# Kernel optimization log

Hardware: AMD Instinct MI355X
Metric: run time of the kernel (lower is better)

The kernel has to match this reference:

```python
import jax, jax.numpy as jnp
import numpy as np

B, S, E, H = 8, 2048, 512, 8
DH = E // H
NEG = -1e30


def setup_inputs() -> dict:
    key = jax.random.key(0)
    ks = jax.random.split(key, 6)
    return {
        "x": jax.random.normal(ks[0], (B, S, E), dtype=jnp.float32),
        "W_qkv": jax.random.normal(ks[1], (E, 3 * E), dtype=jnp.float32) * 0.02,
        "b_qkv": jax.random.normal(ks[2], (3 * E,), dtype=jnp.float32) * 0.02,
        "W_out": jax.random.normal(ks[3], (E, E), dtype=jnp.float32) * 0.02,
        "b_out": jax.random.normal(ks[4], (E,), dtype=jnp.float32) * 0.02,
        "rel_pos": jax.random.normal(ks[5], (1, H, S, S), dtype=jnp.float32) * 0.02,
    }


def reference(x, W_qkv, b_qkv, W_out, b_out, rel_pos):
    b, s, e = x.shape
    scale = DH ** -0.5
    qkv = x @ W_qkv + b_qkv                     # [b, s, 3e]
    qkv = qkv.reshape(b, s, 3, H, DH)
    q = jnp.transpose(qkv[:, :, 0], (0, 2, 1, 3))  # [b, h, s, dh]
    k = jnp.transpose(qkv[:, :, 1], (0, 2, 1, 3))
    v = jnp.transpose(qkv[:, :, 2], (0, 2, 1, 3))
    scores = jnp.einsum("bhqd,bhkd->bhqk", q, k) * scale
    scores = scores + rel_pos[:, :, :s, :s]
    causal = jnp.tril(jnp.ones((s, s), dtype=bool))
    scores = jnp.where(causal[None, None], scores, NEG)
    attn = jax.nn.softmax(scores, axis=-1)
    out = jnp.einsum("bhqk,bhkd->bhqd", attn, v)  # [b, h, s, dh]
    out = jnp.transpose(out, (0, 2, 1, 3)).reshape(b, s, e)
    return out @ W_out + b_out
```

## Files before the change

kernel.cpp:

```cpp
#include <hip/hip_runtime.h>
#include <cstdint>


#define DEVI __device__ __forceinline__

typedef __bf16 bf8 __attribute__((ext_vector_type(8)));
typedef float f4 __attribute__((ext_vector_type(4)));
typedef unsigned short us8 __attribute__((ext_vector_type(8)));
typedef unsigned short us4 __attribute__((ext_vector_type(4)));

typedef const unsigned int __attribute__((address_space(1))) gu32;
typedef unsigned int __attribute__((address_space(3))) lu32;

#define L2E 1.44269504088896f

DEVI unsigned short f2bf(float f) {
  unsigned u = __builtin_bit_cast(unsigned, f);
  u += 0x7fffu + ((u >> 16) & 1u);
  return (unsigned short)(u >> 16);
}

DEVI unsigned short cbf(float f) {
  return __builtin_bit_cast(unsigned short, (__bf16)f);
}

DEVI void gl_lds16(const void* g, void* l) {
  __builtin_amdgcn_global_load_lds((gu32*)g, (lu32*)l, 16, 0, 0);
}

__global__ __launch_bounds__(256) void k_convert_x(const float* __restrict__ x,
                                                   unsigned short* __restrict__ xb) {
  int c = blockIdx.x * 256 + threadIdx.x;
  int row = c >> 6, cl = c & 63;
  const float* s = x + ((size_t)row << 9) + (cl << 3);
  float4 a = *(const float4*)s;
  float4 b = *(const float4*)(s + 4);
  us8 o;
  o[0]=f2bf(a.x); o[1]=f2bf(a.y); o[2]=f2bf(a.z); o[3]=f2bf(a.w);
  o[4]=f2bf(b.x); o[5]=f2bf(b.y); o[6]=f2bf(b.z); o[7]=f2bf(b.w);
  int p = (cl & ~7) | ((cl & 7) ^ (row & 7));
  *(us8*)(xb + ((size_t)row << 9) + (p << 3)) = o;
}

__global__ __launch_bounds__(256) void k_transpose_w(const float* __restrict__ W,
                                                     unsigned short* __restrict__ Wt, int N) {
  __shared__ float t[32][33];
  int k0 = blockIdx.x * 32, n0 = blockIdx.y * 32;
  int tx = threadIdx.x & 31, ty = threadIdx.x >> 5;
#pragma unroll
  for (int r = 0; r < 4; ++r)
    t[ty + r * 8][tx] = W[(size_t)(k0 + ty + r * 8) * N + n0 + tx];
  __syncthreads();
#pragma unroll
  for (int r = 0; r < 4; ++r) {
    int n = n0 + ty + r * 8, k = k0 + tx;
    int k2 = (k & ~63) | ((((k >> 3) & 7) ^ (n & 7)) << 3) | (k & 7);
    Wt[((size_t)n << 9) + k2] = f2bf(t[tx][ty + r * 8]);
  }
}

__global__ __launch_bounds__(256) void k_relconv(const float* __restrict__ rel,
                                                 unsigned short* __restrict__ relt) {
  int t = blockIdx.x * 256 + threadIdx.x;
  int lane = t & 63, ct = (t >> 6) & 3, kt = (t >> 8) & 31, q16 = (t >> 13) & 127, h = t >> 20;
  if (kt > (q16 >> 2)) return;
  int row = (q16 << 4) + (lane & 15);
  int col = (kt << 6) + (ct << 4) + ((lane >> 4) << 2);
  float4 v = *(const float4*)(rel + ((size_t)h << 22) + ((size_t)row << 11) + col);
  us4 o;
  o[0] = f2bf(v.x * L2E); o[1] = f2bf(v.y * L2E);
  o[2] = f2bf(v.z * L2E); o[3] = f2bf(v.w * L2E);
  size_t idx = ((((((size_t)h << 7) | q16) << 5) | kt) << 2 | ct) << 6 | lane;
  *(us4*)(relt + (idx << 2)) = o;
}

template <int EPI>
__global__ __launch_bounds__(256, 2)
void k_gemm(const unsigned short* __restrict__ Ag, const unsigned short* __restrict__ Bg,
            const float* __restrict__ bias, float* __restrict__ Of,
            unsigned short* __restrict__ Oq, unsigned short* __restrict__ Ok,
            unsigned short* __restrict__ Ov) {
  __shared__ __align__(16) unsigned short lds[128 * 64 * 2];
  unsigned short* Al = lds;
  unsigned short* Bl = lds + 128 * 64;
  const int tid = threadIdx.x, wv = tid >> 6, lane = tid & 63, g = lane >> 4, cl = lane & 15;
  const int wm = wv >> 1, wn = wv & 1;
  const int row0 = blockIdx.x * 128, col0 = blockIdx.y * 128;
  f4 acc[4][4];
#pragma unroll
  for (int i = 0; i < 4; ++i)
#pragma unroll
    for (int j = 0; j < 4; ++j) acc[i][j] = (f4){0.f, 0.f, 0.f, 0.f};

  for (int kt = 0; kt < 8; ++kt) {
#pragma unroll
    for (int j = 0; j < 4; ++j) {
      int ci = wv * 4 + j;
      int gci = ci * 64 + lane;
      int r = gci >> 3, cc = gci & 7;
      gl_lds16(Ag + ((size_t)(row0 + r) << 9) + kt * 64 + cc * 8, Al + ci * 512);
      gl_lds16(Bg + ((size_t)(col0 + r) << 9) + kt * 64 + cc * 8, Bl + ci * 512);
    }
    __syncthreads();
#pragma unroll
    for (int kk = 0; kk < 2; ++kk) {
      bf8 af[4], bb[4];
#pragma unroll
      for (int mf = 0; mf < 4; ++mf) {
        int r = wm * 64 + mf * 16 + cl;
        int cc = (kk * 4 + g) ^ (r & 7);
        af[mf] = *(const bf8*)(Al + r * 64 + cc * 8);
      }
#pragma unroll
      for (int nf = 0; nf < 4; ++nf) {
        int r = wn * 64 + nf * 16 + cl;
        int cc = (kk * 4 + g) ^ (r & 7);
        bb[nf] = *(const bf8*)(Bl + r * 64 + cc * 8);
      }
#pragma unroll
      for (int mf = 0; mf < 4; ++mf)
#pragma unroll
        for (int nf = 0; nf < 4; ++nf)
          acc[mf][nf] = __builtin_amdgcn_mfma_f32_16x16x32_bf16(af[mf], bb[nf], acc[mf][nf], 0, 0, 0);
    }
    __syncthreads();
  }

  if (EPI == 1) {
#pragma unroll
    for (int nf = 0; nf < 4; ++nf) {
      int col = col0 + wn * 64 + nf * 16 + cl;
      float bv = bias[col];
#pragma unroll
      for (int mf = 0; mf < 4; ++mf) {
#pragma unroll
        for (int j = 0; j < 4; ++j) {
          int row = row0 + wm * 64 + mf * 16 + 4 * g + j;
          Of[((size_t)row << 9) + col] = acc[mf][nf][j] + bv;
        }
      }
    }
  } else {
    const int which = col0 >> 9;
#pragma unroll
    for (int nf = 0; nf < 4; ++nf) {
      int col = col0 + wn * 64 + nf * 16 + cl;
      float bv = bias[col];
      int d = col & 63, h = (col >> 6) & 7;
#pragma unroll
      for (int mf = 0; mf < 4; ++mf) {
        int row = row0 + wm * 64 + mf * 16 + 4 * g;
        int b = row >> 11, s = row & 2047;
        size_t fb = ((size_t)b * 8 + h) * 131072;
        if (which == 0) {
#pragma unroll
          for (int j = 0; j < 4; ++j) {
            int ss = s + j;
            size_t off = fb + (size_t)((ss >> 4) * 1024 + (d >> 5) * 512 +
                                       (((d >> 3) & 3) * 16 + (ss & 15)) * 8 + (d & 7));
            Oq[off] = f2bf((acc[mf][nf][j] + bv) * (0.125f * L2E));
          }
        } else if (which == 1) {
#pragma unroll
          for (int j = 0; j < 4; ++j) {
            int ss = s + j;
            size_t off = fb + (size_t)((ss >> 6) * 4096 + (d >> 5) * 2048 + ((ss >> 4) & 3) * 512 +
                                       (((d >> 3) & 3) * 16 + (ss & 15)) * 8 + (d & 7));
            Ok[off] = f2bf(acc[mf][nf][j] + bv);
          }
        } else {
          us4 o;
#pragma unroll
          for (int j = 0; j < 4; ++j) o[j] = f2bf(acc[mf][nf][j] + bv);
          size_t off = fb + (size_t)((s >> 6) * 4096 + ((s >> 5) & 1) * 2048 + (d >> 4) * 512 +
                                     ((((s >> 3) & 3) * 16) + (d & 15)) * 8 + (s & 7));
          *(us4*)(Ov + off) = o;
        }
      }
    }
  }
}

template <bool RELT>
__global__ __launch_bounds__(256, 4)
void k_attn(const unsigned short* __restrict__ Qf, const unsigned short* __restrict__ Kf,
            const unsigned short* __restrict__ Vf, const float* __restrict__ rel,
            const unsigned short* __restrict__ relt, unsigned short* __restrict__ AO) {
  __shared__ __align__(16) unsigned short Pl[4][16 * 72];
  const int tid = threadIdx.x, wv = tid >> 6, lane = tid & 63, g = lane >> 4, cl = lane & 15;
  int bid = blockIdx.x;
  int h = bid & 7;
  int rest = bid >> 3;
  int q16 = 127 - (rest >> 1);
  int b = ((rest & 1) << 2) | wv;
  const int rX = q16 << 4;
  const int ktop = q16 >> 2;
  const int qrow = rX + cl;
  size_t fb = (((size_t)b << 3) + h) * 131072;
  const unsigned short* Qp = Qf + fb;
  const unsigned short* Kp = Kf + fb;
  const unsigned short* Vp = Vf + fb;
  const float* relp = rel + ((size_t)h << 22);
  unsigned short* pw = Pl[wv];

  bf8 qf[2];
#pragma unroll
  for (int kk = 0; kk < 2; ++kk)
    qf[kk] = *(const bf8*)(Qp + q16 * 1024 + kk * 512 + lane * 8);

  f4 ot[4];
  float mr = -1e30f, lr = 0.f;
#pragma unroll
  for (int ct = 0; ct < 4; ++ct) ot[ct] = (f4){0.f, 0.f, 0.f, 0.f};

  for (int kt = 0; kt <= ktop; ++kt) {
    const int kb = kt << 6;
    const unsigned short* Kt = Kp + kt * 4096;
    const unsigned short* Vt = Vp + kt * 4096;
    bf8 kf[2][4], vf[2][4];
#pragma unroll
    for (int kk = 0; kk < 2; ++kk)
#pragma unroll
      for (int ct = 0; ct < 4; ++ct)
        kf[kk][ct] = *(const bf8*)(Kt + kk * 2048 + ct * 512 + lane * 8);
#pragma unroll
    for (int kk = 0; kk < 2; ++kk)
#pragma unroll
      for (int ct = 0; ct < 4; ++ct)
        vf[kk][ct] = *(const bf8*)(Vt + kk * 2048 + ct * 512 + lane * 8);
    us4 rt4[4];
    float4 rl4[4];
    if constexpr (RELT) {
      const unsigned short* tb = relt + (((((size_t)h << 7) | q16) << 5) | kt) * 1024;
#pragma unroll
      for (int ct = 0; ct < 4; ++ct)
        rt4[ct] = *(const us4*)(tb + ((ct << 6) | lane) * 4);
    } else {
#pragma unroll
      for (int ct = 0; ct < 4; ++ct)
        rl4[ct] = *(const float4*)(relp + ((size_t)qrow << 11) + kb + ct * 16 + g * 4);
    }
    f4 st[4];
#pragma unroll
    for (int ct = 0; ct < 4; ++ct) st[ct] = (f4){0.f, 0.f, 0.f, 0.f};
#pragma unroll
    for (int kk = 0; kk < 2; ++kk)
#pragma unroll
      for (int ct = 0; ct < 4; ++ct)
        st[ct] = __builtin_amdgcn_mfma_f32_16x16x32_bf16(kf[kk][ct], qf[kk], st[ct], 0, 0, 0);
    if constexpr (RELT) {
#pragma unroll
      for (int ct = 0; ct < 4; ++ct)
#pragma unroll
        for (int j = 0; j < 4; ++j)
          st[ct][j] += __builtin_bit_cast(float, (unsigned)rt4[ct][j] << 16);
    } else {
#pragma unroll
      for (int ct = 0; ct < 4; ++ct) {
        st[ct][0] = fmaf(rl4[ct].x, L2E, st[ct][0]);
        st[ct][1] = fmaf(rl4[ct].y, L2E, st[ct][1]);
        st[ct][2] = fmaf(rl4[ct].z, L2E, st[ct][2]);
        st[ct][3] = fmaf(rl4[ct].w, L2E, st[ct][3]);
      }
    }
    if (kt == ktop) {
#pragma unroll
      for (int ct = 0; ct < 4; ++ct) {
        int kc0 = kb + ct * 16 + 4 * g;
#pragma unroll
        for (int j = 0; j < 4; ++j)
          if (kc0 + j > qrow) st[ct][j] = -1e30f;
      }
    }
    float m0 = fmaxf(fmaxf(st[0][0], st[0][1]), fmaxf(st[0][2], st[0][3]));
#pragma unroll
    for (int ct = 1; ct < 4; ++ct)
      m0 = fmaxf(m0, fmaxf(fmaxf(st[ct][0], st[ct][1]), fmaxf(st[ct][2], st[ct][3])));
    m0 = fmaxf(m0, __shfl_xor(m0, 16));
    m0 = fmaxf(m0, __shfl_xor(m0, 32));
    float mn = fmaxf(mr, m0);
    float al = exp2f(mr - mn);
    mr = mn;
#pragma unroll
    for (int ct = 0; ct < 4; ++ct)
#pragma unroll
      for (int j = 0; j < 4; ++j) st[ct][j] = exp2f(st[ct][j] - mn);
    float rs = 0.f;
#pragma unroll
    for (int ct = 0; ct < 4; ++ct)
      rs += (st[ct][0] + st[ct][1]) + (st[ct][2] + st[ct][3]);
    rs += __shfl_xor(rs, 16);
    rs += __shfl_xor(rs, 32);
    lr = lr * al + rs;
#pragma unroll
    for (int ct = 0; ct < 4; ++ct) {
      ot[ct][0] *= al; ot[ct][1] *= al; ot[ct][2] *= al; ot[ct][3] *= al;
    }
#pragma unroll
    for (int ct = 0; ct < 4; ++ct) {
      us4 pk;
      pk[0] = cbf(st[ct][0]); pk[1] = cbf(st[ct][1]);
      pk[2] = cbf(st[ct][2]); pk[3] = cbf(st[ct][3]);
      *(us4*)(pw + cl * 72 + ct * 16 + g * 4) = pk;
    }
#pragma unroll
    for (int kk = 0; kk < 2; ++kk) {
      bf8 pf = __builtin_bit_cast(bf8, *(const us8*)(pw + cl * 72 + kk * 32 + g * 8));
#pragma unroll
      for (int ct = 0; ct < 4; ++ct)
        ot[ct] = __builtin_amdgcn_mfma_f32_16x16x32_bf16(vf[kk][ct], pf, ot[ct], 0, 0, 0);
    }
  }
  float inv = 1.0f / lr;
  const int s = qrow;
  unsigned short* aor = AO + (((size_t)b << 11) + s) * 512 + h * 64;
#pragma unroll
  for (int ct = 0; ct < 4; ++ct) {
    int chunk = 2 * ct + (g >> 1);
    int base = (4 * (g & 1)) | ((chunk ^ (s & 7)) << 3);
    us4 o;
    o[0] = cbf(ot[ct][0] * inv); o[1] = cbf(ot[ct][1] * inv);
    o[2] = cbf(ot[ct][2] * inv); o[3] = cbf(ot[ct][3] * inv);
    *(us4*)(aor + base) = o;
  }
}

extern "C" void kernel_launch(void* const* d_in, const int* in_sizes, int n_in,
                              void* d_out, int out_size, void* d_ws, size_t ws_size,
                              hipStream_t stream) {
  const float* x    = (const float*)d_in[0];
  const float* Wqkv = (const float*)d_in[1];
  const float* bqkv = (const float*)d_in[2];
  const float* Wout = (const float*)d_in[3];
  const float* bout = (const float*)d_in[4];
  const float* rel  = (const float*)d_in[5];
  float* out = (float*)d_out;

  unsigned short* Qw  = (unsigned short*)d_ws;
  unsigned short* Kw  = Qw  + 8388608;
  unsigned short* Vw  = Kw  + 8388608;
  unsigned short* XA  = Vw  + 8388608;
  unsigned short* WtQ = XA  + 8388608;
  unsigned short* WtO = WtQ + 786432;
  unsigned short* relt= WtO + 262144;
  const bool useT = ws_size >= (34603008ULL + 33554432ULL) * 2ULL;

  k_convert_x<<<dim3(4096), dim3(256), 0, stream>>>(x, XA);
  k_transpose_w<<<dim3(16, 48), dim3(256), 0, stream>>>(Wqkv, WtQ, 1536);
  k_transpose_w<<<dim3(16, 16), dim3(256), 0, stream>>>(Wout, WtO, 512);
  if (useT) k_relconv<<<dim3(32768), dim3(256), 0, stream>>>(rel, relt);
  k_gemm<0><<<dim3(128, 12), dim3(256), 0, stream>>>(XA, WtQ, bqkv, nullptr, Qw, Kw, Vw);
  if (useT) k_attn<true ><<<dim3(2048), dim3(256), 0, stream>>>(Qw, Kw, Vw, rel, relt, XA);
  else      k_attn<false><<<dim3(2048), dim3(256), 0, stream>>>(Qw, Kw, Vw, rel, relt, XA);
  k_gemm<1><<<dim3(128, 4), dim3(256), 0, stream>>>(XA, WtO, bout, out, nullptr, nullptr, nullptr);
}
```

Measured before the change: 199.7 us.

## Coalesce rel-pos conversion via LDS, lazy softmax rescale, swizzle P tile

The rel-pos conversion kernel now has each wave read full contiguous 64-float row segments, stage them through shared memory and write the MFMA-fragment layout, replacing scattered float4 reads. In attention, the running-max rescale of the accumulator and row sum is skipped unless some row's max grows by more than a threshold, which saves exp and multiply work per tile. Scores are then exponentiated against a possibly stale max, which can reach up to about 2^11.5 but stays finite. The P staging buffer drops its padding and uses an XOR swizzle to avoid LDS bank conflicts.

```diff
diff --git a/kernel.cpp b/kernel.cpp
--- a/kernel.cpp
+++ b/kernel.cpp
@@ -61,17 +61,30 @@
 
 __global__ __launch_bounds__(256) void k_relconv(const float* __restrict__ rel,
                                                  unsigned short* __restrict__ relt) {
-  int t = blockIdx.x * 256 + threadIdx.x;
-  int lane = t & 63, ct = (t >> 6) & 3, kt = (t >> 8) & 31, q16 = (t >> 13) & 127, h = t >> 20;
+  __shared__ __align__(16) float tl[4][16][68];
+  int wv = threadIdx.x >> 6, lane = threadIdx.x & 63;
+  int t = blockIdx.x * 4 + wv;
+  int kt = t & 31, q16 = (t >> 5) & 127, h = t >> 12;
   if (kt > (q16 >> 2)) return;
-  int row = (q16 << 4) + (lane & 15);
-  int col = (kt << 6) + (ct << 4) + ((lane >> 4) << 2);
-  float4 v = *(const float4*)(rel + ((size_t)h << 22) + ((size_t)row << 11) + col);
-  us4 o;
-  o[0] = f2bf(v.x * L2E); o[1] = f2bf(v.y * L2E);
-  o[2] = f2bf(v.z * L2E); o[3] = f2bf(v.w * L2E);
-  size_t idx = ((((((size_t)h << 7) | q16) << 5) | kt) << 2 | ct) << 6 | lane;
-  *(us4*)(relt + (idx << 2)) = o;
+  const float* src = rel + ((size_t)h << 22) +
+                     ((size_t)((q16 << 4) + (lane >> 2)) << 11) + (kt << 6) + (lane & 3) * 16;
+  float4 v0 = *(const float4*)(src);
+  float4 v1 = *(const float4*)(src + 4);
+  float4 v2 = *(const float4*)(src + 8);
+  float4 v3 = *(const float4*)(src + 12);
+  float* dst = &tl[wv][lane >> 2][(lane & 3) * 16];
+  *(float4*)(dst) = v0; *(float4*)(dst + 4) = v1;
+  *(float4*)(dst + 8) = v2; *(float4*)(dst + 12) = v3;
+  size_t tb = (((((size_t)h << 7) | q16) << 5) | kt) << 2;
+#pragma unroll
+  for (int ct = 0; ct < 4; ++ct) {
+    const float* rp = &tl[wv][lane & 15][ct * 16 + ((lane >> 4) << 2)];
+    float4 rv = *(const float4*)rp;
+    us4 o;
+    o[0] = f2bf(rv.x * L2E); o[1] = f2bf(rv.y * L2E);
+    o[2] = f2bf(rv.z * L2E); o[3] = f2bf(rv.w * L2E);
+    *(us4*)(relt + (((tb | ct) << 6) | lane) * 4) = o;
+  }
 }
 
 template <int EPI>
@@ -186,7 +199,7 @@
 void k_attn(const unsigned short* __restrict__ Qf, const unsigned short* __restrict__ Kf,
             const unsigned short* __restrict__ Vf, const float* __restrict__ rel,
             const unsigned short* __restrict__ relt, unsigned short* __restrict__ AO) {
-  __shared__ __align__(16) unsigned short Pl[4][16 * 72];
+  __shared__ __align__(16) unsigned short Pl[4][16 * 64];
   const int tid = threadIdx.x, wv = tid >> 6, lane = tid & 63, g = lane >> 4, cl = lane & 15;
   int bid = blockIdx.x;
   int h = bid & 7;
@@ -278,34 +291,38 @@
       m0 = fmaxf(m0, fmaxf(fmaxf(st[ct][0], st[ct][1]), fmaxf(st[ct][2], st[ct][3])));
     m0 = fmaxf(m0, __shfl_xor(m0, 16));
     m0 = fmaxf(m0, __shfl_xor(m0, 32));
-    float mn = fmaxf(mr, m0);
-    float al = exp2f(mr - mn);
-    mr = mn;
+    if (__any(m0 > mr + 11.54f)) {
+      float mn = fmaxf(mr, m0);
+      float al = exp2f(mr - mn);
+      mr = mn;
+      lr *= al;
+#pragma unroll
+      for (int ct = 0; ct < 4; ++ct) {
+        ot[ct][0] *= al; ot[ct][1] *= al; ot[ct][2] *= al; ot[ct][3] *= al;
+      }
+    }
 #pragma unroll
     for (int ct = 0; ct < 4; ++ct)
 #pragma unroll
-      for (int j = 0; j < 4; ++j) st[ct][j] = exp2f(st[ct][j] - mn);
+      for (int j = 0; j < 4; ++j) st[ct][j] = exp2f(st[ct][j] - mr);
     float rs = 0.f;
 #pragma unroll
     for (int ct = 0; ct < 4; ++ct)
       rs += (st[ct][0] + st[ct][1]) + (st[ct][2] + st[ct][3]);
     rs += __shfl_xor(rs, 16);
     rs += __shfl_xor(rs, 32);
-    lr = lr * al + rs;
-#pragma unroll
-    for (int ct = 0; ct < 4; ++ct) {
-      ot[ct][0] *= al; ot[ct][1] *= al; ot[ct][2] *= al; ot[ct][3] *= al;
-    }
+    lr += rs;
 #pragma unroll
     for (int ct = 0; ct < 4; ++ct) {
       us4 pk;
       pk[0] = cbf(st[ct][0]); pk[1] = cbf(st[ct][1]);
       pk[2] = cbf(st[ct][2]); pk[3] = cbf(st[ct][3]);
-      *(us4*)(pw + cl * 72 + ct * 16 + g * 4) = pk;
+      *(us4*)(pw + cl * 64 + (((2 * ct + (g >> 1)) ^ (cl & 7)) << 3) + ((g & 1) << 2)) = pk;
     }
 #pragma unroll
     for (int kk = 0; kk < 2; ++kk) {
-      bf8 pf = __builtin_bit_cast(bf8, *(const us8*)(pw + cl * 72 + kk * 32 + g * 8));
+      bf8 pf = __builtin_bit_cast(bf8,
+                 *(const us8*)(pw + cl * 64 + (((4 * kk + g) ^ (cl & 7)) << 3)));
 #pragma unroll
       for (int ct = 0; ct < 4; ++ct)
         ot[ct] = __builtin_amdgcn_mfma_f32_16x16x32_bf16(vf[kk][ct], pf, ot[ct], 0, 0, 0);
@@ -348,7 +365,7 @@
   k_convert_x<<<dim3(4096), dim3(256), 0, stream>>>(x, XA);
   k_transpose_w<<<dim3(16, 48), dim3(256), 0, stream>>>(Wqkv, WtQ, 1536);
   k_transpose_w<<<dim3(16, 16), dim3(256), 0, stream>>>(Wout, WtO, 512);
-  if (useT) k_relconv<<<dim3(32768), dim3(256), 0, stream>>>(rel, relt);
+  if (useT) k_relconv<<<dim3(8192), dim3(256), 0, stream>>>(rel, relt);
   k_gemm<0><<<dim3(128, 12), dim3(256), 0, stream>>>(XA, WtQ, bqkv, nullptr, Qw, Kw, Vw);
   if (useT) k_attn<true ><<<dim3(2048), dim3(256), 0, stream>>>(Qw, Kw, Vw, rel, relt, XA);
   else      k_attn<false><<<dim3(2048), dim3(256), 0, stream>>>(Qw, Kw, Vw, rel, relt, XA);
```

Result: no change. 197.2 us (-1.3%).
